# Optimization experiments

Measured on AMD Instinct MI355X. Metric: run time of the kernel, lower is better.

Reference implementation:

```python
import jax, jax.numpy as jnp
import numpy as np

FP = 2048       # fingerprint / hopf_input_size
A = 1024        # hopf_asso_dim (num_heads = 1)
B = 512         # batch of molecules
T = 50000       # number of templates (memory size)
BETA = 0.125    # hopf_beta


def setup_inputs() -> dict:
    key = jax.random.key(0)
    k_m, k_t, k_wm, k_wt = jax.random.split(key, 4)
    # binary-ish fingerprints approximated with uniform [0,1)
    m = jax.random.uniform(k_m, (B, FP), dtype=jnp.float32)
    templates = jax.random.uniform(k_t, (T, FP), dtype=jnp.float32)
    # kaiming_normal fan_in linear: std = 1/sqrt(fan_in)
    std = 1.0 / np.sqrt(FP)
    W_mol = jax.random.normal(k_wm, (A, FP), dtype=jnp.float32) * std
    b_mol = jnp.zeros((A,), dtype=jnp.float32)
    W_temp = jax.random.normal(k_wt, (A, FP), dtype=jnp.float32) * std
    b_temp = jnp.zeros((A,), dtype=jnp.float32)
    return {"m": m, "templates": templates, "W_mol": W_mol, "b_mol": b_mol,
            "W_temp": W_temp, "b_temp": b_temp}


def reference(m, templates, W_mol, b_mol, W_temp, b_temp):
    # mol encoder: single Linear (last layer -> no activation, dropout=0 eval)
    Xi = m @ W_mol.T + b_mol                 # [B, A] queries
    # template encoder: single Linear -> stored pattern memory
    X = templates @ W_temp.T + b_temp       # [T, A] keys/memory
    # Hopfield association: beta-scaled similarity = logits over templates
    out = BETA * jnp.einsum('ba,ta->bt', Xi, X)   # [B, T]
    return out
```

## Files before the change

kernel.cpp:

```cpp
#include <hip/hip_runtime.h>
#include <cstdint>
#include <cstddef>

typedef __attribute__((ext_vector_type(8))) short short8;
typedef __attribute__((ext_vector_type(8))) _Float16 f16x8;
typedef __attribute__((ext_vector_type(4))) float f32x4;
typedef __attribute__((ext_vector_type(4))) unsigned short u16x4;
typedef unsigned short u16;

#define FP_  2048
#define AD_  1024
#define BB_  512
#define TT_  50000
#define BETA_ 0.125f

__device__ __forceinline__ u16 f2bf(float x){
  uint32_t u = __builtin_bit_cast(uint32_t, x);
  u = (u + 0x7fffu + ((u >> 16) & 1u)) >> 16;
  return (u16)u;
}
__device__ __forceinline__ float bf2f(u16 h){
  uint32_t u = ((uint32_t)h) << 16;
  return __builtin_bit_cast(float, u);
}
__device__ __forceinline__ u16 f2h_bits(float x){
  _Float16 h = (_Float16)x;
  return __builtin_bit_cast(u16, h);
}
__device__ __forceinline__ unsigned int pkrtz_u32(float a, float b){
  return __builtin_bit_cast(unsigned int, __builtin_amdgcn_cvt_pkrtz(a, b));
}

__device__ __forceinline__ void gload_lds16(const void* g, void* l){
  __builtin_amdgcn_global_load_lds((const __attribute__((address_space(1))) void*)g,
                                   (__attribute__((address_space(3))) void*)l,
                                   16, 0, 0);
}

#define SB   __builtin_amdgcn_s_barrier()
#define SCH  __builtin_amdgcn_sched_barrier(0)
#define WAIT_LGKM0 asm volatile("s_waitcnt lgkmcnt(0)" ::: "memory")
#define WAIT_VM(n) asm volatile("s_waitcnt vmcnt(" #n ")" ::: "memory")

__global__ void conv_hilo_k(const float* __restrict__ src, u16* __restrict__ hi,
                            u16* __restrict__ lo, int n){
  int i = (blockIdx.x * blockDim.x + threadIdx.x) * 4;
  if (i >= n) return;
  f32x4 v = *reinterpret_cast<const f32x4*>(src + i);
  u16x4 h, l;
  #pragma unroll
  for (int e = 0; e < 4; ++e){
    float x = v[e];
    u16 hs = f2bf(x);
    h[e] = hs;
    l[e] = f2bf(x - bf2f(hs));
  }
  *reinterpret_cast<u16x4*>(hi + i) = h;
  *reinterpret_cast<u16x4*>(lo + i) = l;
}

__global__ void conv_hilo_T_k(const float* __restrict__ W, u16* __restrict__ hiT,
                              u16* __restrict__ loT, int R, int C){
  __shared__ float tile[32][33];
  int c0 = blockIdx.x * 32;
  int r0 = blockIdx.y * 32;
  int tx = threadIdx.x;
  int ty = threadIdx.y;
  #pragma unroll
  for (int i = 0; i < 32; i += 8)
    tile[ty + i][tx] = W[(size_t)(r0 + ty + i) * C + c0 + tx];
  __syncthreads();
  #pragma unroll
  for (int i = 0; i < 32; i += 8){
    float x = tile[tx][ty + i];
    u16 hs = f2bf(x);
    size_t o = (size_t)(c0 + ty + i) * R + r0 + tx;
    hiT[o] = hs;
    loT[o] = f2bf(x - bf2f(hs));
  }
}

__global__ void dot_rows_k(const float* __restrict__ Xi, const float* __restrict__ bt,
                           float* __restrict__ c, int K){
  int row  = blockIdx.x * 4 + (threadIdx.x >> 6);
  int lane = threadIdx.x & 63;
  float s = 0.f;
  for (int a = lane; a < K; a += 64) s += Xi[(size_t)row * K + a] * bt[a];
  #pragma unroll
  for (int off = 32; off; off >>= 1) s += __shfl_down(s, off);
  if (lane == 0) c[row] = s;
}

template<int TM, int TN, int FM, int FN, int OUT16>
__global__ __launch_bounds__(256, 2)
void gemm_hilo(const u16* __restrict__ Ahi, const u16* __restrict__ Alo,
               const u16* __restrict__ Bhi, const u16* __restrict__ Blo,
               int M, int N, int K,
               float* __restrict__ Cf, u16* __restrict__ Chi, u16* __restrict__ Clo,
               const float* __restrict__ colBias)
{
  constexpr int BK = 32;
  constexpr int WM = TM / (16 * FM);
  constexpr int WN = TN / (16 * FN);
  static_assert(WM * WN == 4, "4 waves / 256 threads");
  constexpr int BUFE = (2 * TM + 2 * TN) * BK;

  __shared__ __align__(16) u16 lds[2 * BUFE];

  const int m0 = blockIdx.x * TM;
  const int n0 = blockIdx.y * TN;

  const int tid  = threadIdx.x;
  const int w    = tid >> 6;
  const int lane = tid & 63;
  const int lr   = lane & 15;
  const int lg   = lane >> 4;
  const int wm   = w / WN;
  const int wn   = w % WN;

  const int rrA = tid >> 2;
  const int chA = tid & 3;

  short8 ra[2], rb[2];

  f32x4 acc[FM][FN];
  #pragma unroll
  for (int i = 0; i < FM; ++i)
    #pragma unroll
    for (int j = 0; j < FN; ++j)
      acc[i][j] = (f32x4){0.f, 0.f, 0.f, 0.f};

  auto stage_load = [&](int k0){
    int gm = m0 + rrA;
    ra[0] = *reinterpret_cast<const short8*>(Ahi + (size_t)gm * K + k0 + chA * 8);
    ra[1] = *reinterpret_cast<const short8*>(Alo + (size_t)gm * K + k0 + chA * 8);
    int gn = n0 + rrA; if (gn > N - 1) gn = N - 1;
    rb[0] = *reinterpret_cast<const short8*>(Bhi + (size_t)gn * K + k0 + chA * 8);
    rb[1] = *reinterpret_cast<const short8*>(Blo + (size_t)gn * K + k0 + chA * 8);
  };
  auto stage_store = [&](int buf){
    u16* As_hi = lds + buf * BUFE;
    u16* As_lo = As_hi + TM * BK;
    u16* Bs_hi = As_hi + 2 * TM * BK;
    u16* Bs_lo = As_hi + 2 * TM * BK + TN * BK;
    int row = rrA;
    int sw  = (chA ^ ((row >> 1) & 3)) << 3;
    *reinterpret_cast<short8*>(As_hi + row * BK + sw) = ra[0];
    *reinterpret_cast<short8*>(As_lo + row * BK + sw) = ra[1];
    *reinterpret_cast<short8*>(Bs_hi + row * BK + sw) = rb[0];
    *reinterpret_cast<short8*>(Bs_lo + row * BK + sw) = rb[1];
  };

  const int NT = K / BK;
  stage_load(0);
  stage_store(0);
  __syncthreads();

  int cur = 0;
  for (int t = 0; t < NT; ++t){
    const bool have_next = (t + 1 < NT);
    if (have_next) stage_load((t + 1) * BK);

    u16* As_hi = lds + cur * BUFE;
    u16* As_lo = As_hi + TM * BK;
    u16* Bs_hi = As_hi + 2 * TM * BK;
    u16* Bs_lo = As_hi + 2 * TM * BK + TN * BK;

    short8 ah[FM], al[FM], bh[FN], bl[FN];
    #pragma unroll
    for (int i = 0; i < FM; ++i){
      int row = wm * FM * 16 + i * 16 + lr;
      int off = row * BK + ((lg ^ ((row >> 1) & 3)) << 3);
      ah[i] = *reinterpret_cast<short8*>(As_hi + off);
      al[i] = *reinterpret_cast<short8*>(As_lo + off);
    }
    #pragma unroll
    for (int j = 0; j < FN; ++j){
      int row = wn * FN * 16 + j * 16 + lr;
      int off = row * BK + ((lg ^ ((row >> 1) & 3)) << 3);
      bh[j] = *reinterpret_cast<short8*>(Bs_hi + off);
      bl[j] = *reinterpret_cast<short8*>(Bs_lo + off);
    }
    #pragma unroll
    for (int i = 0; i < FM; ++i)
      #pragma unroll
      for (int j = 0; j < FN; ++j){
        acc[i][j] = __builtin_amdgcn_mfma_f32_16x16x32_bf16(ah[i], bh[j], acc[i][j], 0, 0, 0);
        acc[i][j] = __builtin_amdgcn_mfma_f32_16x16x32_bf16(ah[i], bl[j], acc[i][j], 0, 0, 0);
        acc[i][j] = __builtin_amdgcn_mfma_f32_16x16x32_bf16(al[i], bh[j], acc[i][j], 0, 0, 0);
      }

    if (have_next){
      __builtin_amdgcn_sched_barrier(0);
      stage_store(cur ^ 1);
      __syncthreads();
    }
    cur ^= 1;
  }

  #pragma unroll
  for (int i = 0; i < FM; ++i){
    int rbase = m0 + wm * FM * 16 + i * 16 + lg * 4;
    #pragma unroll
    for (int j = 0; j < FN; ++j){
      int gcol = n0 + wn * FN * 16 + j * 16 + lr;
      if (gcol < N){
        float cb = colBias ? colBias[gcol] : 0.f;
        #pragma unroll
        for (int r = 0; r < 4; ++r){
          int grow = rbase + r;
          float v = acc[i][j][r] + cb;
          size_t idx = (size_t)grow * N + gcol;
          if (Cf) Cf[idx] = v;
          if constexpr (OUT16 == 1){
            u16 hs = f2bf(v);
            Chi[idx] = hs;
            Clo[idx] = f2bf(v - bf2f(hs));
          } else if constexpr (OUT16 == 2){
            _Float16 h = (_Float16)v;
            Chi[idx] = __builtin_bit_cast(u16, h);
            Clo[idx] = f2h_bits(v - (float)h);
          }
        }
      }
    }
  }
}

__global__ __launch_bounds__(512, 1)
void gemm_big(const u16* __restrict__ Ah,
              const float* __restrict__ Bf,
              float* __restrict__ C,
              const float* __restrict__ rowAdd, float alpha)
{
  constexpr int K = FP_, NN = TT_;
  constexpr int NT = K / 64;
  constexpr int KS = 8192;
  constexpr int BOFF = 16384;
  constexpr int SLOT = 32768;

  __shared__ __align__(16) u16 lds[2 * SLOT];

  int id  = blockIdx.x;
  int xcd = id & 7;
  int g   = id >> 3;
  int mt  = g & 1;
  int sg  = g >> 1;
  int strips = (xcd < 4) ? 25 : 24;
  if (sg >= strips) return;
  int nt = ((xcd < 4) ? xcd * 25 : 100 + (xcd - 4) * 24) + sg;
  const int m0 = mt * 256;
  const int n0 = nt * 256;

  const int tid  = threadIdx.x;
  const int w    = tid >> 6;
  const int lane = tid & 63;
  const int lr   = lane & 15;
  const int lg   = lane >> 4;
  const int wm   = w >> 2;
  const int wn   = w & 3;

  auto glA = [&](u16* sp_, int Tt, int h){
    int rl = lane >> 2;
    int cc = lane & 3;
    int row = h * 128 + w * 16 + rl;
    #pragma unroll
    for (int ks = 0; ks < 2; ++ks){
      const u16* src = Ah + (size_t)(m0 + row) * K + Tt * 64 + ks * 32
                     + ((cc ^ ((row >> 1) & 3)) << 3);
      gload_lds16(src, sp_ + ks * KS + (size_t)(h * 128 + w * 16) * 32);
    }
  };
  auto issueB = [&](int Tt, int h, f32x4 (&rb)[4]){
    #pragma unroll
    for (int p = 0; p < 4; ++p){
      int rl = h * 128 + p * 32 + (tid >> 4);
      int gn = n0 + rl; if (gn > NN - 1) gn = NN - 1;
      rb[p] = *reinterpret_cast<const f32x4*>(Bf + (size_t)gn * K + Tt * 64 + (tid & 15) * 4);
    }
  };
  auto publishB = [&](u16* sp_, int h, f32x4 (&rb)[4]){
    int fch = tid & 15;
    int ks  = fch >> 3;
    int c16 = (fch & 7) >> 1;
    int hf  = fch & 1;
    #pragma unroll
    for (int p = 0; p < 4; ++p){
      int row = h * 128 + p * 32 + (tid >> 4);
      uint2 hv;
      hv.x = pkrtz_u32(rb[p][0], rb[p][1]);
      hv.y = pkrtz_u32(rb[p][2], rb[p][3]);
      int phys = c16 ^ ((row >> 1) & 3);
      *reinterpret_cast<uint2*>(sp_ + BOFF + ks * KS + row * 32 + phys * 8 + hf * 4) = hv;
    }
  };

  f32x4 acc[8][4];
  #pragma unroll
  for (int i = 0; i < 8; ++i)
    #pragma unroll
    for (int j = 0; j < 4; ++j)
      acc[i][j] = (f32x4){0.f, 0.f, 0.f, 0.f};

  f32x4 rbB0[4], rbB1[4];
  f16x8 pa[4][2], pb[2][2];

#define READ_FRAGS(SP, MH, NH)                                                 \
  _Pragma("unroll")                                                            \
  for (int ii = 0; ii < 4; ++ii){                                              \
    int row_ = wm * 128 + ((MH) * 4 + ii) * 16 + lr;                           \
    _Pragma("unroll")                                                          \
    for (int ks_ = 0; ks_ < 2; ++ks_)                                          \
      pa[ii][ks_] = __builtin_bit_cast(f16x8, *reinterpret_cast<short8*>(      \
        (SP) + ks_ * KS + row_ * 32 + ((lg ^ ((row_ >> 1) & 3)) << 3)));       \
  }                                                                            \
  _Pragma("unroll")                                                            \
  for (int jj = 0; jj < 2; ++jj){                                              \
    int row_ = wn * 64 + ((NH) * 2 + jj) * 16 + lr;                            \
    _Pragma("unroll")                                                          \
    for (int ks_ = 0; ks_ < 2; ++ks_)                                          \
      pb[jj][ks_] = __builtin_bit_cast(f16x8, *reinterpret_cast<short8*>(      \
        (SP) + BOFF + ks_ * KS + row_ * 32 + ((lg ^ ((row_ >> 1) & 3)) << 3)));\
  }

#define MMA(MH, NH)                                                            \
  __builtin_amdgcn_s_setprio(1);                                               \
  _Pragma("unroll")                                                            \
  for (int ii = 0; ii < 4; ++ii)                                               \
    _Pragma("unroll")                                                          \
    for (int jj = 0; jj < 2; ++jj){                                            \
      acc[(MH)*4+ii][(NH)*2+jj] = __builtin_amdgcn_mfma_f32_16x16x32_f16(      \
          pa[ii][0], pb[jj][0], acc[(MH)*4+ii][(NH)*2+jj], 0, 0, 0);           \
      acc[(MH)*4+ii][(NH)*2+jj] = __builtin_amdgcn_mfma_f32_16x16x32_f16(      \
          pa[ii][1], pb[jj][1], acc[(MH)*4+ii][(NH)*2+jj], 0, 0, 0);           \
    }                                                                          \
  __builtin_amdgcn_s_setprio(0);

  glA(lds, 0, 0);  glA(lds, 0, 1);
  SCH;
  issueB(0, 0, rbB0);
  issueB(0, 1, rbB1);
  SCH;
  WAIT_VM(4); SCH;
  publishB(lds, 0, rbB0);
  WAIT_VM(0); SCH;
  publishB(lds, 1, rbB1);
  SCH;
  issueB(1, 0, rbB0);
  issueB(1, 1, rbB1);
  WAIT_LGKM0;
  SB; SCH;

  for (int T = 0; T < NT; ++T){
    u16* sp  = lds + (size_t)(T & 1) * SLOT;
    u16* spn = lds + (size_t)((T + 1) & 1) * SLOT;
    const bool hasN  = (T + 1 < NT);
    const bool hasNN = (T + 2 < NT);

    READ_FRAGS(sp, 0, 0);
    if (hasN) glA(spn, T + 1, 0);
    SB; WAIT_LGKM0; SCH;
    MMA(0, 0);
    SB;

    READ_FRAGS(sp, 0, 1);
    if (hasN){
      glA(spn, T + 1, 1);
      SCH;
      WAIT_VM(8); SCH;
      publishB(spn, 0, rbB0);
      if (hasNN){ issueB(T + 2, 0, rbB0); SCH; }
    }
    SB; WAIT_LGKM0; SCH;
    MMA(0, 1);
    SB;

    READ_FRAGS(sp, 1, 0);
    if (hasN){
      if (hasNN) { WAIT_VM(8); } else { WAIT_VM(4); }
      SCH;
      publishB(spn, 1, rbB1);
      if (hasNN){ issueB(T + 2, 1, rbB1); SCH; }
    }
    SB; WAIT_LGKM0; SCH;
    MMA(1, 0);
    SB;

    READ_FRAGS(sp, 1, 1);
    if (hasN){
      if (hasNN) { WAIT_VM(8); } else { WAIT_VM(0); }
      SCH;
    }
    SB; WAIT_LGKM0; SCH;
    MMA(1, 1);
    SB;
  }

#undef READ_FRAGS
#undef MMA

  #pragma unroll
  for (int i = 0; i < 8; ++i){
    int rbase = m0 + wm * 128 + i * 16 + lg * 4;
    #pragma unroll
    for (int j = 0; j < 4; ++j){
      int gcol = n0 + wn * 64 + j * 16 + lr;
      if (gcol < NN){
        #pragma unroll
        for (int r = 0; r < 4; ++r){
          int grow = rbase + r;
          float v = (acc[i][j][r] + rowAdd[grow]) * alpha;
          C[(size_t)grow * NN + gcol] = v;
        }
      }
    }
  }
}

extern "C" void kernel_launch(void* const* d_in, const int* in_sizes, int n_in,
                              void* d_out, int out_size, void* d_ws, size_t ws_size,
                              hipStream_t stream){
  (void)in_sizes; (void)n_in; (void)out_size; (void)ws_size;
  const float* m    = (const float*)d_in[0];
  const float* tpl  = (const float*)d_in[1];
  const float* Wmol = (const float*)d_in[2];
  const float* bmol = (const float*)d_in[3];
  const float* Wtmp = (const float*)d_in[4];
  const float* btmp = (const float*)d_in[5];
  float* out = (float*)d_out;

  uint8_t* wp = (uint8_t*)d_ws;
  auto carve = [&](size_t bytes) -> void* {
    void* p = (void*)wp;
    wp += (bytes + 255) & ~(size_t)255;
    return p;
  };
  u16* m_hi   = (u16*)carve((size_t)BB_ * FP_ * 2);
  u16* m_lo   = (u16*)carve((size_t)BB_ * FP_ * 2);
  u16* wm_hi  = (u16*)carve((size_t)AD_ * FP_ * 2);
  u16* wm_lo  = (u16*)carve((size_t)AD_ * FP_ * 2);
  u16* wtT_hi = (u16*)carve((size_t)FP_ * AD_ * 2);
  u16* wtT_lo = (u16*)carve((size_t)FP_ * AD_ * 2);
  float* Xi   = (float*)carve((size_t)BB_ * AD_ * 4);
  u16* Xi_hi  = (u16*)carve((size_t)BB_ * AD_ * 2);
  u16* Xi_lo  = (u16*)carve((size_t)BB_ * AD_ * 2);
  u16* Y_hi   = (u16*)carve((size_t)BB_ * FP_ * 2);
  u16* Y_lo   = (u16*)carve((size_t)BB_ * FP_ * 2);
  float* cvec = (float*)carve((size_t)BB_ * 4);

  conv_hilo_k<<<(BB_ * FP_ / 4 + 255) / 256, 256, 0, stream>>>(m, m_hi, m_lo, BB_ * FP_);
  conv_hilo_k<<<(AD_ * FP_ / 4 + 255) / 256, 256, 0, stream>>>(Wmol, wm_hi, wm_lo, AD_ * FP_);
  conv_hilo_T_k<<<dim3(FP_ / 32, AD_ / 32), dim3(32, 8), 0, stream>>>(Wtmp, wtT_hi, wtT_lo, AD_, FP_);

  gemm_hilo<64, 64, 2, 2, 1><<<dim3(BB_ / 64, AD_ / 64), 256, 0, stream>>>(
      m_hi, m_lo, wm_hi, wm_lo, BB_, AD_, FP_,
      Xi, Xi_hi, Xi_lo, bmol);

  dot_rows_k<<<BB_ / 4, 256, 0, stream>>>(Xi, btmp, cvec, AD_);

  gemm_hilo<64, 64, 2, 2, 2><<<dim3(BB_ / 64, FP_ / 64), 256, 0, stream>>>(
      Xi_hi, Xi_lo, wtT_hi, wtT_lo, BB_, FP_, AD_,
      nullptr, Y_hi, Y_lo, nullptr);

  gemm_big<<<400, 512, 0, stream>>>(Y_hi, tpl, out, cvec, BETA_);
}
```

Measured before the change: 256.9 us.

## Shrink big GEMM tile to 256x128 with K=32 steps for higher occupancy

```diff
diff --git a/kernel.cpp b/kernel.cpp
--- a/kernel.cpp
+++ b/kernel.cpp
@@ -227,17 +227,16 @@
   }
 }
 
-__global__ __launch_bounds__(512, 1)
+__global__ __launch_bounds__(512, 4)
 void gemm_big(const u16* __restrict__ Ah,
               const float* __restrict__ Bf,
               float* __restrict__ C,
               const float* __restrict__ rowAdd, float alpha)
 {
   constexpr int K = FP_, NN = TT_;
-  constexpr int NT = K / 64;
-  constexpr int KS = 8192;
-  constexpr int BOFF = 16384;
-  constexpr int SLOT = 32768;
+  constexpr int NT = K / 32;
+  constexpr int BOFF = 8192;
+  constexpr int SLOT = 12288;
 
   __shared__ __align__(16) u16 lds[2 * SLOT];
 
@@ -245,163 +244,146 @@
   int xcd = id & 7;
   int g   = id >> 3;
   int mt  = g & 1;
-  int sg  = g >> 1;
-  int strips = (xcd < 4) ? 25 : 24;
-  if (sg >= strips) return;
-  int nt = ((xcd < 4) ? xcd * 25 : 100 + (xcd - 4) * 24) + sg;
+  int s   = g >> 1;
+  int strips = (xcd < 7) ? 49 : 48;
+  if (s >= strips) return;
+  int nt = ((xcd < 7) ? xcd * 49 : 343) + s;
   const int m0 = mt * 256;
-  const int n0 = nt * 256;
+  const int n0 = nt * 128;
 
   const int tid  = threadIdx.x;
   const int w    = tid >> 6;
   const int lane = tid & 63;
   const int lr   = lane & 15;
   const int lg   = lane >> 4;
-  const int wm   = w >> 2;
-  const int wn   = w & 3;
-
-  auto glA = [&](u16* sp_, int Tt, int h){
+  const int wm   = w >> 1;
+  const int wn   = w & 1;
+
+  auto glA = [&](int Tt, u16* sp_){
     int rl = lane >> 2;
     int cc = lane & 3;
-    int row = h * 128 + w * 16 + rl;
-    #pragma unroll
-    for (int ks = 0; ks < 2; ++ks){
-      const u16* src = Ah + (size_t)(m0 + row) * K + Tt * 64 + ks * 32
+    #pragma unroll
+    for (int q = 0; q < 2; ++q){
+      int row = w * 32 + q * 16 + rl;
+      const u16* src = Ah + (size_t)(m0 + row) * K + Tt * 32
                      + ((cc ^ ((row >> 1) & 3)) << 3);
-      gload_lds16(src, sp_ + ks * KS + (size_t)(h * 128 + w * 16) * 32);
-    }
-  };
-  auto issueB = [&](int Tt, int h, f32x4 (&rb)[4]){
-    #pragma unroll
-    for (int p = 0; p < 4; ++p){
-      int rl = h * 128 + p * 32 + (tid >> 4);
-      int gn = n0 + rl; if (gn > NN - 1) gn = NN - 1;
-      rb[p] = *reinterpret_cast<const f32x4*>(Bf + (size_t)gn * K + Tt * 64 + (tid & 15) * 4);
-    }
-  };
-  auto publishB = [&](u16* sp_, int h, f32x4 (&rb)[4]){
-    int fch = tid & 15;
-    int ks  = fch >> 3;
-    int c16 = (fch & 7) >> 1;
-    int hf  = fch & 1;
-    #pragma unroll
-    for (int p = 0; p < 4; ++p){
-      int row = h * 128 + p * 32 + (tid >> 4);
+      gload_lds16(src, sp_ + (size_t)(w * 32 + q * 16) * 32);
+    }
+  };
+  const int rowB = tid >> 2;
+  const int c4   = tid & 3;
+  auto issueB = [&](int Tt, f32x4 (&rb)[2]){
+    int gn = n0 + rowB; if (gn > NN - 1) gn = NN - 1;
+    const float* base = Bf + (size_t)gn * K + Tt * 32;
+    rb[0] = *reinterpret_cast<const f32x4*>(base + c4 * 4);
+    rb[1] = *reinterpret_cast<const f32x4*>(base + (c4 + 4) * 4);
+  };
+  auto publishB = [&](u16* sp_, f32x4 (&rb)[2]){
+    u16* bb = sp_ + BOFF;
+    int swr = (rowB >> 1) & 3;
+    #pragma unroll
+    for (int p = 0; p < 2; ++p){
+      int lc = (c4 + p * 4) >> 1;
+      int hf = c4 & 1;
       uint2 hv;
       hv.x = pkrtz_u32(rb[p][0], rb[p][1]);
       hv.y = pkrtz_u32(rb[p][2], rb[p][3]);
-      int phys = c16 ^ ((row >> 1) & 3);
-      *reinterpret_cast<uint2*>(sp_ + BOFF + ks * KS + row * 32 + phys * 8 + hf * 4) = hv;
-    }
-  };
-
-  f32x4 acc[8][4];
-  #pragma unroll
-  for (int i = 0; i < 8; ++i)
+      int phys = lc ^ swr;
+      *reinterpret_cast<uint2*>(bb + rowB * 32 + phys * 8 + hf * 4) = hv;
+    }
+  };
+
+  f32x4 acc[4][4];
+  #pragma unroll
+  for (int i = 0; i < 4; ++i)
     #pragma unroll
     for (int j = 0; j < 4; ++j)
       acc[i][j] = (f32x4){0.f, 0.f, 0.f, 0.f};
 
-  f32x4 rbB0[4], rbB1[4];
-  f16x8 pa[4][2], pb[2][2];
-
-#define READ_FRAGS(SP, MH, NH)                                                 \
+  f32x4 rbE[2], rbO[2];
+  f16x8 pa[2], pb[2];
+
+#define READ_FRAGS(SP, QM, QN)                                                 \
   _Pragma("unroll")                                                            \
-  for (int ii = 0; ii < 4; ++ii){                                              \
-    int row_ = wm * 128 + ((MH) * 4 + ii) * 16 + lr;                           \
-    _Pragma("unroll")                                                          \
-    for (int ks_ = 0; ks_ < 2; ++ks_)                                          \
-      pa[ii][ks_] = __builtin_bit_cast(f16x8, *reinterpret_cast<short8*>(      \
-        (SP) + ks_ * KS + row_ * 32 + ((lg ^ ((row_ >> 1) & 3)) << 3)));       \
+  for (int ii = 0; ii < 2; ++ii){                                              \
+    int row_ = wm * 64 + ((QM) * 2 + ii) * 16 + lr;                            \
+    pa[ii] = __builtin_bit_cast(f16x8, *reinterpret_cast<short8*>(             \
+      (SP) + row_ * 32 + ((lg ^ ((row_ >> 1) & 3)) << 3)));                    \
   }                                                                            \
   _Pragma("unroll")                                                            \
   for (int jj = 0; jj < 2; ++jj){                                              \
-    int row_ = wn * 64 + ((NH) * 2 + jj) * 16 + lr;                            \
-    _Pragma("unroll")                                                          \
-    for (int ks_ = 0; ks_ < 2; ++ks_)                                          \
-      pb[jj][ks_] = __builtin_bit_cast(f16x8, *reinterpret_cast<short8*>(      \
-        (SP) + BOFF + ks_ * KS + row_ * 32 + ((lg ^ ((row_ >> 1) & 3)) << 3)));\
-  }
-
-#define MMA(MH, NH)                                                            \
+    int row_ = wn * 64 + ((QN) * 2 + jj) * 16 + lr;                            \
+    pb[jj] = __builtin_bit_cast(f16x8, *reinterpret_cast<short8*>(             \
+      (SP) + BOFF + row_ * 32 + ((lg ^ ((row_ >> 1) & 3)) << 3)));             \
+  }
+
+#define MMA(QM, QN)                                                            \
   __builtin_amdgcn_s_setprio(1);                                               \
   _Pragma("unroll")                                                            \
-  for (int ii = 0; ii < 4; ++ii)                                               \
+  for (int ii = 0; ii < 2; ++ii)                                               \
     _Pragma("unroll")                                                          \
-    for (int jj = 0; jj < 2; ++jj){                                            \
-      acc[(MH)*4+ii][(NH)*2+jj] = __builtin_amdgcn_mfma_f32_16x16x32_f16(      \
-          pa[ii][0], pb[jj][0], acc[(MH)*4+ii][(NH)*2+jj], 0, 0, 0);           \
-      acc[(MH)*4+ii][(NH)*2+jj] = __builtin_amdgcn_mfma_f32_16x16x32_f16(      \
-          pa[ii][1], pb[jj][1], acc[(MH)*4+ii][(NH)*2+jj], 0, 0, 0);           \
-    }                                                                          \
+    for (int jj = 0; jj < 2; ++jj)                                             \
+      acc[(QM)*2+ii][(QN)*2+jj] = __builtin_amdgcn_mfma_f32_16x16x32_f16(      \
+          pa[ii], pb[jj], acc[(QM)*2+ii][(QN)*2+jj], 0, 0, 0);                 \
   __builtin_amdgcn_s_setprio(0);
 
-  glA(lds, 0, 0);  glA(lds, 0, 1);
+  glA(0, lds);
   SCH;
-  issueB(0, 0, rbB0);
-  issueB(0, 1, rbB1);
+  issueB(0, rbE);
+  issueB(1, rbO);
   SCH;
-  WAIT_VM(4); SCH;
-  publishB(lds, 0, rbB0);
-  WAIT_VM(0); SCH;
-  publishB(lds, 1, rbB1);
-  SCH;
-  issueB(1, 0, rbB0);
-  issueB(1, 1, rbB1);
+  WAIT_VM(2); SCH;
+  publishB(lds, rbE);
   WAIT_LGKM0;
   SB; SCH;
 
-  for (int T = 0; T < NT; ++T){
+  auto body = [&](int T, f32x4 (&rbFill)[2], f32x4 (&rbPub)[2]){
     u16* sp  = lds + (size_t)(T & 1) * SLOT;
     u16* spn = lds + (size_t)((T + 1) & 1) * SLOT;
     const bool hasN  = (T + 1 < NT);
     const bool hasNN = (T + 2 < NT);
 
     READ_FRAGS(sp, 0, 0);
-    if (hasN) glA(spn, T + 1, 0);
-    SB; WAIT_LGKM0; SCH;
+    if (hasN) glA(T + 1, spn);
+    WAIT_LGKM0; SCH;
     MMA(0, 0);
-    SB;
 
     READ_FRAGS(sp, 0, 1);
-    if (hasN){
-      glA(spn, T + 1, 1);
-      SCH;
-      WAIT_VM(8); SCH;
-      publishB(spn, 0, rbB0);
-      if (hasNN){ issueB(T + 2, 0, rbB0); SCH; }
-    }
-    SB; WAIT_LGKM0; SCH;
+    if (hasNN) issueB(T + 2, rbFill);
+    WAIT_LGKM0; SCH;
     MMA(0, 1);
-    SB;
 
     READ_FRAGS(sp, 1, 0);
     if (hasN){
-      if (hasNN) { WAIT_VM(8); } else { WAIT_VM(4); }
+      if (hasNN) { WAIT_VM(4); } else { WAIT_VM(2); }
       SCH;
-      publishB(spn, 1, rbB1);
-      if (hasNN){ issueB(T + 2, 1, rbB1); SCH; }
-    }
-    SB; WAIT_LGKM0; SCH;
+      publishB(spn, rbPub);
+    }
+    WAIT_LGKM0; SCH;
     MMA(1, 0);
-    SB;
 
     READ_FRAGS(sp, 1, 1);
     if (hasN){
-      if (hasNN) { WAIT_VM(8); } else { WAIT_VM(0); }
+      if (hasNN) { WAIT_VM(2); } else { WAIT_VM(0); }
       SCH;
     }
-    SB; WAIT_LGKM0; SCH;
+    WAIT_LGKM0; SCH;
     MMA(1, 1);
+    SCH;
     SB;
+  };
+
+  for (int tt = 0; tt < NT; tt += 2){
+    body(tt,     rbE, rbO);
+    body(tt + 1, rbO, rbE);
   }
 
 #undef READ_FRAGS
 #undef MMA
 
   #pragma unroll
-  for (int i = 0; i < 8; ++i){
-    int rbase = m0 + wm * 128 + i * 16 + lg * 4;
+  for (int i = 0; i < 4; ++i){
+    int rbase = m0 + wm * 64 + i * 16 + lg * 4;
     #pragma unroll
     for (int j = 0; j < 4; ++j){
       int gcol = n0 + wn * 64 + j * 16 + lr;
@@ -462,5 +444,5 @@
       Xi_hi, Xi_lo, wtT_hi, wtT_lo, BB_, FP_, AD_,
       nullptr, Y_hi, Y_lo, nullptr);
 
-  gemm_big<<<400, 512, 0, stream>>>(Y_hi, tpl, out, cvec, BETA_);
-}
+  gemm_big<<<784, 512, 0, stream>>>(Y_hi, tpl, out, cvec, BETA_);
+}
```

Measured after the change: 276.6 us. +7.7%, slower.
